# Kernel tuning notes

Measured on AMD Instinct MI355X. Metric: run time of the kernel, lower is better.

Reference implementation:

```python
import jax, jax.numpy as jnp
import numpy as np

INPUT_SIZE = 10000
GROUP_SIZE = 500
STEP = GROUP_SIZE // 2            # 250
OUT_PER_GROUP = 50
GROUPS = 2 * INPUT_SIZE // GROUP_SIZE - 1  # 39


def setup_inputs() -> dict:
    key = jax.random.key(0)
    k1, k2 = jax.random.split(key)
    x = jax.random.uniform(k1, (4096, INPUT_SIZE), dtype=jnp.float32)
    # torch init: uniform_(weight, 0.9, 1.1); weight shape per group is [out, in]
    W = jax.random.uniform(k2, (GROUPS, OUT_PER_GROUP, GROUP_SIZE),
                           dtype=jnp.float32, minval=0.9, maxval=1.1)
    return {"x": x, "W": W}


def reference(x, W):
    # gather overlapping windows: idx[g, k] = g*STEP + k  -> [B, GROUPS, GROUP_SIZE]
    idx = jnp.arange(GROUPS)[:, None] * STEP + jnp.arange(GROUP_SIZE)[None, :]
    xw = x[:, idx]                                   # [B, G, K]
    # per-group linear (no bias): out[b,g,o] = sum_k xw[b,g,k] * W[g,o,k]
    out = jnp.einsum('bgk,gok->bgo', xw, W)          # [B, G, O]
    return jax.nn.relu(out.reshape(x.shape[0], GROUPS * OUT_PER_GROUP))
```

## Files before the change

kernel.cpp:

```cpp
#include <hip/hip_runtime.h>
#include <hip/hip_bf16.h>


constexpr int INPUT  = 10000;
constexpr int GROUPS = 39;
constexpr int HALF   = 250;
constexpr int OPG    = 50;
constexpr int OUTW   = 1950;
constexpr int KP     = 512;
constexpr int BMT    = 16;
constexpr int LDH    = 264;
constexpr int SLOT   = BMT * LDH;

__device__ __hip_bfloat16 Wb[GROUPS * OPG * KP];

typedef __attribute__((ext_vector_type(8))) short    short8;
typedef __attribute__((ext_vector_type(4))) float    float4v;
typedef __attribute__((ext_vector_type(2))) unsigned uint2v;

#define LGKM_BAR() do { \
    asm volatile("s_waitcnt lgkmcnt(0)" ::: "memory"); \
    __builtin_amdgcn_sched_barrier(0); \
    __builtin_amdgcn_s_barrier(); \
    __builtin_amdgcn_sched_barrier(0); \
} while (0)

__device__ __forceinline__ unsigned bf2pack(float a, float b) {
    union { float f; unsigned u; } x, y; x.f = a; y.f = b;
    unsigned lo = (x.u + 0x7fffu + ((x.u >> 16) & 1u)) >> 16;
    unsigned hi = (y.u + 0x7fffu + ((y.u >> 16) & 1u)) & 0xffff0000u;
    return hi | lo;
}

__global__ void prep_w(const float* __restrict__ W) {
    const int slot = blockIdx.x * 256 + threadIdx.x;
    if (slot >= GROUPS * OPG * (KP / 2)) return;
    const int go = slot >> 8;
    const int pd = (slot & 255) * 2;
    float2 v = {0.f, 0.f};
    if (pd < 250)                      v = *(const float2*)(W + (size_t)go * 500 + pd);
    else if (pd >= 256 && pd < 506)    v = *(const float2*)(W + (size_t)go * 500 + pd - 6);
    ((unsigned*)Wb)[slot] = bf2pack(v.x, v.y);
}

__global__ __launch_bounds__(256, 4)
void peak_binner_kernel(const float* __restrict__ x,
                        float* __restrict__ out, int batch)
{
    __shared__ __align__(16) short As[4 * SLOT];

    const int my   = blockIdx.x;
    const int gc   = blockIdx.y;
    const int g0   = gc * 10;
    const int NG   = (gc < 3) ? 10 : 9;
    const int tid  = threadIdx.x;
    const int lane = tid & 63;
    const int wave = tid >> 6;
    const int fm   = lane & 15;
    const int l4   = lane >> 4;
    const int nb   = (wave == 3) ? 34 : wave * 16;

    const float* xr0 = x + (size_t)(my * BMT + wave * 4) * INPUT + 4 * lane;
    const __hip_bfloat16* wp = Wb + ((size_t)g0 * OPG + nb + fm) * KP + l4 * 8;

    float4v vS[4];
    short8  bfrag[16];
    float4v acc;

    auto LOADB = [&]() {
        #pragma unroll
        for (int j = 0; j < 16; ++j) bfrag[j] = *(const short8*)(wp + j * 32);
    };

    auto ISSUE = [&](int h) {
        const int gh = g0 + h;
        const float* p0 = xr0 + gh * HALF;
        if (gh != 39) {
            #pragma unroll
            for (int j = 0; j < 4; ++j)
                vS[j] = *(const float4v*)(p0 + (size_t)j * INPUT);
        } else {
            #pragma unroll
            for (int j = 0; j < 4; ++j) {
                if (lane < 62)        vS[j] = *(const float4v*)(p0 + (size_t)j * INPUT);
                else if (lane == 62) { float2 t = *(const float2*)(p0 + (size_t)j * INPUT);
                                       vS[j] = float4v{t.x, t.y, 0.f, 0.f}; }
                else                   vS[j] = float4v{0.f, 0.f, 0.f, 0.f};
            }
        }
    };

    auto CONVERT = [&](int s) {
        #pragma unroll
        for (int j = 0; j < 4; ++j) {
            uint2v w;
            w[0] = bf2pack(vS[j][0], vS[j][1]);
            w[1] = bf2pack(vS[j][2], vS[j][3]);
            *(uint2v*)&As[s * SLOT + (wave * 4 + j) * LDH + 4 * lane] = w;
        }
    };

    auto COMPUTE = [&](int sA, int sB) {
        acc = float4v{0.f, 0.f, 0.f, 0.f};
        const int ab = fm * LDH + l4 * 8;
        __builtin_amdgcn_s_setprio(1);
        #pragma unroll
        for (int kk = 0; kk < 8; ++kk) {
            const short8 a = *(const short8*)&As[sA * SLOT + ab + kk * 32];
            acc = __builtin_amdgcn_mfma_f32_16x16x32_bf16(a, bfrag[kk], acc, 0, 0, 0);
        }
        #pragma unroll
        for (int kk = 0; kk < 8; ++kk) {
            const short8 a = *(const short8*)&As[sB * SLOT + ab + kk * 32];
            acc = __builtin_amdgcn_mfma_f32_16x16x32_bf16(a, bfrag[8 + kk], acc, 0, 0, 0);
        }
        __builtin_amdgcn_s_setprio(0);
    };

    auto EPI = [&](int g) {
        if (wave < 3 || fm >= 14) {
            const int col = g * OPG + nb + fm;
            #pragma unroll
            for (int reg = 0; reg < 4; ++reg)
                out[(size_t)(my * BMT + l4 * 4 + reg) * OUTW + col] = fmaxf(acc[reg], 0.f);
        }
    };

    ISSUE(0); LOADB(); CONVERT(0);
    ISSUE(1); CONVERT(1);
    LGKM_BAR();

    for (int i = 0; i < NG; ++i) {
        if (i + 2 <= NG) ISSUE(i + 2);
        COMPUTE(i & 3, (i + 1) & 3);
        EPI(g0 + i);
        wp += (size_t)OPG * KP;
        if (i + 1 < NG) LOADB();
        if (i + 2 <= NG) CONVERT((i + 2) & 3);
        LGKM_BAR();
    }
}

extern "C" void kernel_launch(void* const* d_in, const int* in_sizes, int n_in,
                              void* d_out, int out_size, void* d_ws, size_t ws_size,
                              hipStream_t stream) {
    const float* x = (const float*)d_in[0];
    const float* W = (const float*)d_in[1];
    float* out     = (float*)d_out;

    const int batch = in_sizes[0] / INPUT;

    const int slots = GROUPS * OPG * (KP / 2);
    prep_w<<<(slots + 255) / 256, 256, 0, stream>>>(W);

    dim3 grid(batch / BMT, 4);
    peak_binner_kernel<<<grid, dim3(256), 0, stream>>>(x, out, batch);
}
```

Measured before the change: 285.1 us.

## Double row tile and double-buffer x and W registers across groups

Each block now handles 32 batch rows, with two accumulators per wave, so every weight fragment loaded from global memory feeds twice as many MFMAs. The x staging and the B-fragment registers are double-buffered and the loop is unrolled by two, issuing x loads three groups ahead on a three-slot LDS ring. Scheduling fences are added to keep the loads ahead of compute. The cost is higher register pressure: launch bounds drop to 2 blocks per SIMD and the grid is half as large, which reduces occupancy and may lower latency hiding.

```diff
diff --git a/kernel.cpp b/kernel.cpp
--- a/kernel.cpp
+++ b/kernel.cpp
@@ -8,7 +8,7 @@
 constexpr int OPG    = 50;
 constexpr int OUTW   = 1950;
 constexpr int KP     = 512;
-constexpr int BMT    = 16;
+constexpr int BMT    = 32;
 constexpr int LDH    = 264;
 constexpr int SLOT   = BMT * LDH;
 
@@ -18,6 +18,7 @@
 typedef __attribute__((ext_vector_type(4))) float    float4v;
 typedef __attribute__((ext_vector_type(2))) unsigned uint2v;
 
+#define FENCE() __builtin_amdgcn_sched_barrier(0)
 #define LGKM_BAR() do { \
     asm volatile("s_waitcnt lgkmcnt(0)" ::: "memory"); \
     __builtin_amdgcn_sched_barrier(0); \
@@ -43,11 +44,11 @@
     ((unsigned*)Wb)[slot] = bf2pack(v.x, v.y);
 }
 
-__global__ __launch_bounds__(256, 4)
+__global__ __launch_bounds__(256, 2)
 void peak_binner_kernel(const float* __restrict__ x,
                         float* __restrict__ out, int batch)
 {
-    __shared__ __align__(16) short As[4 * SLOT];
+    __shared__ __align__(16) short As[3 * SLOT];
 
     const int my   = blockIdx.x;
     const int gc   = blockIdx.y;
@@ -60,59 +61,64 @@
     const int l4   = lane >> 4;
     const int nb   = (wave == 3) ? 34 : wave * 16;
 
-    const float* xr0 = x + (size_t)(my * BMT + wave * 4) * INPUT + 4 * lane;
+    const float* xr0 = x + (size_t)(my * BMT + wave * 8) * INPUT + 4 * lane;
     const __hip_bfloat16* wp = Wb + ((size_t)g0 * OPG + nb + fm) * KP + l4 * 8;
 
-    float4v vS[4];
-    short8  bfrag[16];
-    float4v acc;
+    float4v vS0[8], vS1[8];
+    short8  bfA[16], bfB[16];
+    float4v acc0, acc1;
 
-    auto LOADB = [&]() {
-        #pragma unroll
-        for (int j = 0; j < 16; ++j) bfrag[j] = *(const short8*)(wp + j * 32);
-    };
-
-    auto ISSUE = [&](int h) {
+    auto ISSUE = [&](int h, float4v* v) {
         const int gh = g0 + h;
         const float* p0 = xr0 + gh * HALF;
         if (gh != 39) {
             #pragma unroll
-            for (int j = 0; j < 4; ++j)
-                vS[j] = *(const float4v*)(p0 + (size_t)j * INPUT);
+            for (int j = 0; j < 8; ++j)
+                v[j] = *(const float4v*)(p0 + (size_t)j * INPUT);
         } else {
             #pragma unroll
-            for (int j = 0; j < 4; ++j) {
-                if (lane < 62)        vS[j] = *(const float4v*)(p0 + (size_t)j * INPUT);
+            for (int j = 0; j < 8; ++j) {
+                if (lane < 62)        v[j] = *(const float4v*)(p0 + (size_t)j * INPUT);
                 else if (lane == 62) { float2 t = *(const float2*)(p0 + (size_t)j * INPUT);
-                                       vS[j] = float4v{t.x, t.y, 0.f, 0.f}; }
-                else                   vS[j] = float4v{0.f, 0.f, 0.f, 0.f};
+                                       v[j] = float4v{t.x, t.y, 0.f, 0.f}; }
+                else                   v[j] = float4v{0.f, 0.f, 0.f, 0.f};
             }
         }
     };
 
-    auto CONVERT = [&](int s) {
+    auto LOADB = [&](short8* bf) {
         #pragma unroll
-        for (int j = 0; j < 4; ++j) {
+        for (int j = 0; j < 16; ++j) bf[j] = *(const short8*)(wp + j * 32);
+    };
+
+    auto CONVERT = [&](int s, const float4v* v) {
+        #pragma unroll
+        for (int j = 0; j < 8; ++j) {
             uint2v w;
-            w[0] = bf2pack(vS[j][0], vS[j][1]);
-            w[1] = bf2pack(vS[j][2], vS[j][3]);
-            *(uint2v*)&As[s * SLOT + (wave * 4 + j) * LDH + 4 * lane] = w;
+            w[0] = bf2pack(v[j][0], v[j][1]);
+            w[1] = bf2pack(v[j][2], v[j][3]);
+            *(uint2v*)&As[s * SLOT + (wave * 8 + j) * LDH + 4 * lane] = w;
         }
     };
 
-    auto COMPUTE = [&](int sA, int sB) {
-        acc = float4v{0.f, 0.f, 0.f, 0.f};
+    auto COMPUTE = [&](int sA, int sB, const short8* bf) {
+        acc0 = float4v{0.f, 0.f, 0.f, 0.f};
+        acc1 = float4v{0.f, 0.f, 0.f, 0.f};
         const int ab = fm * LDH + l4 * 8;
         __builtin_amdgcn_s_setprio(1);
         #pragma unroll
         for (int kk = 0; kk < 8; ++kk) {
-            const short8 a = *(const short8*)&As[sA * SLOT + ab + kk * 32];
-            acc = __builtin_amdgcn_mfma_f32_16x16x32_bf16(a, bfrag[kk], acc, 0, 0, 0);
+            const short8 a0 = *(const short8*)&As[sA * SLOT + ab + kk * 32];
+            const short8 a1 = *(const short8*)&As[sA * SLOT + ab + 16 * LDH + kk * 32];
+            acc0 = __builtin_amdgcn_mfma_f32_16x16x32_bf16(a0, bf[kk], acc0, 0, 0, 0);
+            acc1 = __builtin_amdgcn_mfma_f32_16x16x32_bf16(a1, bf[kk], acc1, 0, 0, 0);
         }
         #pragma unroll
         for (int kk = 0; kk < 8; ++kk) {
-            const short8 a = *(const short8*)&As[sB * SLOT + ab + kk * 32];
-            acc = __builtin_amdgcn_mfma_f32_16x16x32_bf16(a, bfrag[8 + kk], acc, 0, 0, 0);
+            const short8 a0 = *(const short8*)&As[sB * SLOT + ab + kk * 32];
+            const short8 a1 = *(const short8*)&As[sB * SLOT + ab + 16 * LDH + kk * 32];
+            acc0 = __builtin_amdgcn_mfma_f32_16x16x32_bf16(a0, bf[8 + kk], acc0, 0, 0, 0);
+            acc1 = __builtin_amdgcn_mfma_f32_16x16x32_bf16(a1, bf[8 + kk], acc1, 0, 0, 0);
         }
         __builtin_amdgcn_s_setprio(0);
     };
@@ -120,24 +126,45 @@
     auto EPI = [&](int g) {
         if (wave < 3 || fm >= 14) {
             const int col = g * OPG + nb + fm;
+            const size_t r0 = (size_t)(my * BMT + l4 * 4) * OUTW + col;
             #pragma unroll
-            for (int reg = 0; reg < 4; ++reg)
-                out[(size_t)(my * BMT + l4 * 4 + reg) * OUTW + col] = fmaxf(acc[reg], 0.f);
+            for (int reg = 0; reg < 4; ++reg) {
+                out[r0 + (size_t)reg * OUTW]        = fmaxf(acc0[reg], 0.f);
+                out[r0 + (size_t)(16 + reg) * OUTW] = fmaxf(acc1[reg], 0.f);
+            }
         }
     };
 
-    ISSUE(0); LOADB(); CONVERT(0);
-    ISSUE(1); CONVERT(1);
+    ISSUE(0, vS0); ISSUE(1, vS1); LOADB(bfA);
+    FENCE();
+    CONVERT(0, vS0); CONVERT(1, vS1);
+    ISSUE(2, vS0);
     LGKM_BAR();
 
-    for (int i = 0; i < NG; ++i) {
-        if (i + 2 <= NG) ISSUE(i + 2);
-        COMPUTE(i & 3, (i + 1) & 3);
-        EPI(g0 + i);
-        wp += (size_t)OPG * KP;
-        if (i + 1 < NG) LOADB();
-        if (i + 2 <= NG) CONVERT((i + 2) & 3);
-        LGKM_BAR();
+    for (int i = 0;; i += 2) {
+        {
+            if (i + 3 <= NG) ISSUE(i + 3, vS1);
+            if (i + 1 < NG) { wp += (size_t)OPG * KP; LOADB(bfB); }
+            FENCE();
+            COMPUTE(i % 3, (i + 1) % 3, bfA);
+            EPI(g0 + i);
+            FENCE();
+            if (i + 2 <= NG) CONVERT((i + 2) % 3, vS0);
+            LGKM_BAR();
+        }
+        if (i + 1 >= NG) break;
+        {
+            const int k = i + 1;
+            if (k + 3 <= NG) ISSUE(k + 3, vS0);
+            if (k + 1 < NG) { wp += (size_t)OPG * KP; LOADB(bfA); }
+            FENCE();
+            COMPUTE(k % 3, (k + 1) % 3, bfB);
+            EPI(g0 + k);
+            FENCE();
+            if (k + 2 <= NG) CONVERT((k + 2) % 3, vS1);
+            LGKM_BAR();
+        }
+        if (i + 2 >= NG) break;
     }
 }
 
@@ -153,6 +180,6 @@
     const int slots = GROUPS * OPG * (KP / 2);
     prep_w<<<(slots + 255) / 256, 256, 0, stream>>>(W);
 
-    dim3 grid(batch / BMT, 4);
+    dim3 grid((batch + BMT - 1) / BMT, 4);
     peak_binner_kernel<<<grid, dim3(256), 0, stream>>>(x, out, batch);
 }
```

After: 272.0 us. -4.6%, faster.
